# Kernel optimization log

Hardware: AMD Instinct MI355X
Metric: run time of the kernel (lower is better)

The kernel has to match this reference:

```python
import jax, jax.numpy as jnp
import numpy as np

N, C, WP, H, W = 2, 64, 64, 240, 320
NB, K = 6, 3  # num_bases, input_ks
EPS = 1e-5


def _conv(x, w, pad):
    return jax.lax.conv_general_dilated(
        x, w, (1, 1), [(pad, pad), (pad, pad)],
        dimension_numbers=('NCHW', 'OIHW', 'NCHW'))


def _bn(x, g, b, m, v):
    # eval-mode BatchNorm2d with running stats
    inv = g * jax.lax.rsqrt(v + EPS)
    return x * inv[None, :, None, None] + (b - m * inv)[None, :, None, None]


def _forward(feat, weight, w1, b1, w2, b2, coef, coef_bias,
             br_gamma, br_beta, br_mean, br_var,
             w3, bn3_gamma, bn3_beta, bn3_mean, bn3_var):
    n, c, h, w = feat.shape
    # conv_bases: Basic2d (3x3 conv + bias + relu) then 1x1 conv -> K*K*NB channels
    cat = jnp.concatenate([feat, weight], axis=1)
    t = jax.nn.relu(_conv(cat, w1, 1) + b1[None, :, None, None])
    bases = _conv(t, w2, 0) + b2[None, :, None, None]          # [N, NB*K*K, H, W]
    bases = bases.reshape(n, NB, K * K, h, w)                   # [N, NB, L, H, W]
    # F.unfold: im2col patches, channel-major (C outer, kh*kw inner) like torch
    patches = jax.lax.conv_general_dilated_patches(
        feat, (K, K), (1, 1), [(1, 1), (1, 1)],
        dimension_numbers=('NCHW', 'OIHW', 'NCHW'))             # [N, C*K*K, H, W]
    patches = patches.reshape(n, c, K * K, h, w)                # [N, C, L, H, W]
    # dynamic per-pixel basis combination
    bases_out = jnp.einsum('bmlhw,bclhw->bcmhw', bases, patches)
    bases_out = bases_out.reshape(n, c * NB, h, w)              # [N, C*NB, H, W]
    # 1x1 conv with coef + bias
    out = _conv(bases_out, coef, 0) + coef_bias[None, :, None, None]
    # br: BN + ReLU
    out = jax.nn.relu(_bn(out, br_gamma, br_beta, br_mean, br_var))
    # conv3: Basic2d with BN (3x3 conv no bias + BN + ReLU)
    out = _conv(out, w3, 1)
    out = jax.nn.relu(_bn(out, bn3_gamma, bn3_beta, bn3_mean, bn3_var))
    return out


def setup_inputs() -> dict:
    key = jax.random.key(0)
    ks = jax.random.split(key, 8)
    f = lambda i, s, sc: jax.random.normal(ks[i], s, dtype=jnp.float32) * sc
    return {
        'feat': f(0, (N, C, H, W), 1.0),
        'weight': f(1, (N, WP, H, W), 1.0),
        'w1': f(2, (C, C + WP, 3, 3), 0.05),
        'b1': jnp.zeros((C,), jnp.float32),
        'w2': f(3, (K * K * NB, C, 1, 1), 0.05),
        'b2': jnp.zeros((K * K * NB,), jnp.float32),
        'coef': f(4, (C, C * NB, 1, 1), 0.05),
        'coef_bias': jnp.zeros((C,), jnp.float32),
        'br_gamma': jnp.ones((C,), jnp.float32),
        'br_beta': jnp.zeros((C,), jnp.float32),
        'br_mean': jnp.zeros((C,), jnp.float32),
        'br_var': jnp.ones((C,), jnp.float32),
        'w3': f(5, (C, C, 3, 3), 0.05),
        'bn3_gamma': jnp.ones((C,), jnp.float32),
        'bn3_beta': jnp.zeros((C,), jnp.float32),
        'bn3_mean': jnp.zeros((C,), jnp.float32),
        'bn3_var': jnp.ones((C,), jnp.float32),
    }


def reference(feat, weight, w1, b1, w2, b2, coef, coef_bias,
              br_gamma, br_beta, br_mean, br_var,
              w3, bn3_gamma, bn3_beta, bn3_mean, bn3_var):
    return _forward(feat, weight, w1, b1, w2, b2, coef, coef_bias,
                    br_gamma, br_beta, br_mean, br_var,
                    w3, bn3_gamma, bn3_beta, bn3_mean, bn3_var)
```

## Files before the change

### kernel.cpp

```cpp
#include <hip/hip_runtime.h>
#include <math.h>

#define HH 240
#define WW 320
#define HWSZ (240*320)
#define NN 2

#define OFF_BW1   0
#define OFF_BW3   147456
#define OFF_W2A   221184
#define OFF_COEFA 229376
#define OFF_BN    278528
#define OFF_FHF   279552
#define OFF_FHW   19940352

typedef __attribute__((ext_vector_type(8))) _Float16 half8v;
typedef __attribute__((ext_vector_type(4))) _Float16 half4v;
typedef __attribute__((ext_vector_type(2))) _Float16 half2v;
typedef __attribute__((ext_vector_type(4))) float f32x4;

__device__ __forceinline__ half8v h8zero() {
    half8v z;
    #pragma unroll
    for (int j = 0; j < 8; ++j) z[j] = (_Float16)0.f;
    return z;
}

__device__ void do_prep(int id, const float* __restrict__ w1, const float* __restrict__ w3,
                        const float* __restrict__ w2, const float* __restrict__ coef,
                        const float* __restrict__ coef_bias,
                        const float* __restrict__ brg, const float* __restrict__ brb,
                        const float* __restrict__ brm, const float* __restrict__ brv,
                        const float* __restrict__ g3, const float* __restrict__ b3,
                        const float* __restrict__ m3, const float* __restrict__ v3,
                        float* __restrict__ ws) {
    _Float16* hw = (_Float16*)ws;

    if (id < 9216) {
        int l = id & 63; int f = id >> 6;
        int m = f & 3;   int g = f >> 2;
        int t = g % 9, cc = g / 9;
        _Float16* dst = hw + OFF_BW1/2 + (size_t)(g*4 + m)*512 + l*8;
        #pragma unroll
        for (int j = 0; j < 8; ++j) {
            int ci = cc*32 + (l>>4)*8 + j;
            int co = m*16 + (l&15);
            dst[j] = (_Float16)w1[(co*128 + ci)*9 + t];
        }
        return;
    }
    id -= 9216;
    if (id < 4608) {
        int l = id & 63; int f = id >> 6;
        int m = f & 3;   int g = f >> 2;
        int t = g % 9, cc = g / 9;
        _Float16* dst = hw + OFF_BW3/2 + (size_t)(g*4 + m)*512 + l*8;
        #pragma unroll
        for (int j = 0; j < 8; ++j) {
            int ci = cc*32 + (l>>4)*8 + j;
            int co = m*16 + (l&15);
            dst[j] = (_Float16)w3[(co*64 + ci)*9 + t];
        }
        return;
    }
    id -= 4608;
    if (id < 512) {
        int l = id & 63; int f = id >> 6;
        int mf = f & 3, kc = f >> 2;
        int row = mf*16 + (l & 15);
        _Float16* dst = hw + OFF_W2A/2 + (size_t)((kc*4 + mf)*64 + l)*8;
        #pragma unroll
        for (int j = 0; j < 8; ++j) {
            int k = kc*32 + (l>>4)*8 + j;
            dst[j] = (row < 54) ? (_Float16)w2[row*64 + k] : (_Float16)0.f;
        }
        return;
    }
    id -= 512;
    if (id < 3072) {
        int l = id & 63; int f = id >> 6;
        int ocf = f & 3; int g2 = f >> 2;
        int ch = g2 % 3, cg = g2 / 3;
        int oc = ocf*16 + (l & 15);
        _Float16* dst = hw + OFF_COEFA/2 + (size_t)((g2*4 + ocf)*64 + l)*8;
        #pragma unroll
        for (int j = 0; j < 8; ++j) {
            int k32 = (l>>4)*8 + j;
            int m = ch*2 + (k32 >> 4);
            int c = cg*16 + (k32 & 15);
            dst[j] = (_Float16)coef[oc*384 + c*6 + m];
        }
        return;
    }
    id -= 3072;
    if (id < 64) {
        float s = brg[id] * rsqrtf(brv[id] + 1e-5f);
        ws[OFF_BN/4 + id]      = s;
        ws[OFF_BN/4 + 64 + id] = coef_bias[id]*s + brb[id] - brm[id]*s;
        return;
    }
    id -= 64;
    if (id < 64) {
        float s = g3[id] * rsqrtf(v3[id] + 1e-5f);
        ws[OFF_BN/4 + 128 + id] = s;
        ws[OFF_BN/4 + 192 + id] = b3[id] - m3[id]*s;
    }
}

__global__ void nhwc_k(const float* __restrict__ feat, const float* __restrict__ wgt,
                       _Float16* __restrict__ fhf, _Float16* __restrict__ fhw,
                       const float* __restrict__ w1, const float* __restrict__ w3,
                       const float* __restrict__ w2, const float* __restrict__ coef,
                       const float* __restrict__ coef_bias,
                       const float* __restrict__ brg, const float* __restrict__ brb,
                       const float* __restrict__ brm, const float* __restrict__ brv,
                       const float* __restrict__ g3, const float* __restrict__ b3,
                       const float* __restrict__ m3, const float* __restrict__ v3,
                       float* __restrict__ ws) {
    __shared__ float L[64][65];
    const int tid = threadIdx.x;

    const int bid = blockIdx.y * 5 + blockIdx.x;
    if (blockIdx.z == 0 && bid < 69)
        do_prep(bid*256 + tid, w1, w3, w2, coef, coef_bias,
                brg, brb, brm, brv, g3, b3, m3, v3, ws);

    const int xb = blockIdx.x * 64, y = blockIdx.y;
    const int n = blockIdx.z >> 1, w = blockIdx.z & 1;
    const float* src = (w ? wgt : feat) + (size_t)n*64*HWSZ + y*WW + xb;
    _Float16* dst = (w ? fhw : fhf) + ((size_t)n*HWSZ + y*WW + xb) * 64;
    const int lx = tid & 63, c4 = tid >> 6;
    #pragma unroll
    for (int k = 0; k < 16; ++k) {
        int c = c4*16 + k;
        L[c][lx] = src[(size_t)c*HWSZ + lx];
    }
    __syncthreads();
    const int x = tid >> 3, c0 = (tid & 7) * 8;
    #pragma unroll
    for (int h = 0; h < 2; ++h) {
        int xx = x + h*32;
        half8v v;
        #pragma unroll
        for (int j = 0; j < 8; ++j) v[j] = (_Float16)L[c0 + j][xx];
        *(half8v*)&dst[xx*64 + c0] = v;
    }
}

template<int CHUNKS, bool HAS_SCALE>
__launch_bounds__(256, 1)
__global__ void convmfma_k(const _Float16* __restrict__ in0, const _Float16* __restrict__ in1,
                           const _Float16* __restrict__ wfr,
                           const float* __restrict__ epiA, const float* __restrict__ epiB,
                           float* __restrict__ outF, _Float16* __restrict__ outH) {
    __shared__ alignas(16) _Float16 TILE[2][180*40];
    const int tid = threadIdx.x;
    const int lane = tid & 63, wv = tid >> 6;
    const int l15 = lane & 15, l4 = lane >> 4;
    const int x0 = blockIdx.x * 16, y0 = blockIdx.y * 8;
    const int nb = blockIdx.z;
    const int NT = CHUNKS * 9;

    f32x4 acc[8];
    #pragma unroll
    for (int nf = 0; nf < 8; ++nf)
        acc[nf] = (f32x4){0.f, 0.f, 0.f, 0.f};

    half8v sv[3];
    auto issue = [&](int cc) {
        const _Float16* tens = (cc < 2) ? in0 : in1;
        const int choff = (cc & 1) * 32;
        const _Float16* base = tens + (size_t)nb * HWSZ * 64;
        #pragma unroll
        for (int it = 0; it < 3; ++it) {
            int task = tid + it*256;
            sv[it] = h8zero();
            if (it < 2 || task < 720) {
                int pos = task >> 2, hh = task & 3;
                int py = pos / 18, px = pos - py*18;
                int gy = y0 - 1 + py, gx = x0 - 1 + px;
                bool ok = (gy >= 0) & (gy < HH) & (gx >= 0) & (gx < WW);
                if (ok) sv[it] = *(const half8v*)&base[((size_t)(gy*WW + gx))*64 + choff + hh*8];
            }
        }
    };
    auto commit = [&](int buf) {
        #pragma unroll
        for (int it = 0; it < 3; ++it) {
            int task = tid + it*256;
            if (it < 2 || task < 720) {
                int pos = task >> 2, hh = task & 3;
                *(half8v*)&TILE[buf][pos*40 + hh*8] = sv[it];
            }
        }
    };

    half8v Wf[2];
    auto loadW = [&](int g, int b) {
        Wf[b] = *(const half8v*)(wfr + (size_t)(g*4 + wv)*512 + lane*8);
    };

    issue(0);
    commit(0);
    loadW(0, 0);
    __syncthreads();

    #pragma unroll
    for (int cc = 0; cc < CHUNKS; ++cc) {
        if (cc + 1 < CHUNKS) issue(cc + 1);
        const _Float16* Tc = &TILE[cc & 1][0];
        #pragma unroll
        for (int t = 0; t < 9; ++t) {
            const int g = cc*9 + t;
            const int b = g & 1;
            if (g + 1 < NT) loadW(g + 1, b ^ 1);
            const int ky = t / 3, kx = t - ky*3;
            #pragma unroll
            for (int nf = 0; nf < 8; ++nf) {
                int pos = (nf + ky)*18 + l15 + kx;
                half8v Ph = *(const half8v*)&Tc[pos*40 + l4*8];
                acc[nf] = __builtin_amdgcn_mfma_f32_16x16x32_f16(Wf[b], Ph, acc[nf], 0, 0, 0);
            }
        }
        if (cc + 1 < CHUNKS) {
            commit((cc + 1) & 1);
            __syncthreads();
        }
    }

    if (HAS_SCALE) {
        #pragma unroll
        for (int i = 0; i < 4; ++i) {
            int co = wv*16 + l4*4 + i;
            float sc = epiA[co], ofs = epiB[co];
            float* op = outF + (size_t)(nb*64 + co) * HWSZ;
            #pragma unroll
            for (int nf = 0; nf < 8; ++nf) {
                int y = y0 + nf, x = x0 + l15;
                op[y*WW + x] = fmaxf(acc[nf][i]*sc + ofs, 0.f);
            }
        }
    } else {
        #pragma unroll
        for (int nf = 0; nf < 8; ++nf) {
            int y = y0 + nf, x = x0 + l15;
            _Float16* op = outH + ((size_t)nb*HWSZ + y*WW + x) * 64;
            half4v hv;
            #pragma unroll
            for (int i = 0; i < 4; ++i) {
                float v = acc[nf][i] + epiA[wv*16 + l4*4 + i];
                hv[i] = (_Float16)fmaxf(v, 0.f);
            }
            *(half4v*)&op[wv*16 + l4*4] = hv;
        }
    }
}

__launch_bounds__(256, 1)
__global__ void fuse2_k(const _Float16* __restrict__ fhf, const _Float16* __restrict__ tH,
                        const _Float16* __restrict__ w2a,
                        const float* __restrict__ b2,
                        const _Float16* __restrict__ coefa,
                        const float* __restrict__ bn,
                        _Float16* __restrict__ uH) {
    __shared__ alignas(16) _Float16 BSH[128*72];
    __shared__ alignas(16) _Float16 PT[180*24];
    const int tid = threadIdx.x;
    const int lane = tid & 63, wv = tid >> 6;
    const int l15 = lane & 15, l4 = lane >> 4;
    const int x0 = blockIdx.x*16, y0 = blockIdx.y*8;
    const int nb = blockIdx.z;

    int s_pos[2], s_gy[2], s_gx[2], s_oct[2];
    bool s_ok[2], s_act[2];
    #pragma unroll
    for (int it = 0; it < 2; ++it) {
        int task = tid + it*256;
        s_act[it] = (task < 360);
        int pos = task >> 1, oct = task & 1;
        int py = pos / 18, pxx = pos - py*18;
        int gy = y0 - 1 + py, gx = x0 - 1 + pxx;
        s_pos[it] = pos; s_oct[it] = oct;
        s_gy[it] = gy; s_gx[it] = gx;
        s_ok[it] = (gy >= 0) & (gy < HH) & (gx >= 0) & (gx < WW) & s_act[it];
    }
    const _Float16* fbase = fhf + (size_t)nb * HWSZ * 64;

    half8v sv0 = h8zero(), sv1 = h8zero();
    if (s_ok[0]) sv0 = *(const half8v*)&fbase[((size_t)(s_gy[0]*WW + s_gx[0]))*64 + s_oct[0]*8];
    if (s_ok[1]) sv1 = *(const half8v*)&fbase[((size_t)(s_gy[1]*WW + s_gx[1]))*64 + s_oct[1]*8];

    half8v w2f[2][4];
    #pragma unroll
    for (int kc = 0; kc < 2; ++kc)
        #pragma unroll
        for (int mf = 0; mf < 4; ++mf)
            w2f[kc][mf] = *(const half8v*)(w2a + (size_t)((kc*4 + mf)*64 + lane)*8);

    f32x4 b2v[4];
    #pragma unroll
    for (int mf = 0; mf < 4; ++mf)
        #pragma unroll
        for (int i = 0; i < 4; ++i) {
            int row = mf*16 + l4*4 + i;
            b2v[mf][i] = (row < 54) ? b2[row] : 0.f;
        }

    #pragma unroll
    for (int nf = 0; nf < 2; ++nf) {
        int r = wv*2 + nf;
        int y = y0 + r, x = x0 + l15;
        const _Float16* tp = tH + ((size_t)nb*HWSZ + y*WW + x) * 64;
        half8v tf0 = *(const half8v*)&tp[l4*8];
        half8v tf1 = *(const half8v*)&tp[32 + l4*8];
        int px = r*16 + l15;
        #pragma unroll
        for (int mf = 0; mf < 4; ++mf) {
            f32x4 ab = (f32x4){0.f, 0.f, 0.f, 0.f};
            ab = __builtin_amdgcn_mfma_f32_16x16x32_f16(w2f[0][mf], tf0, ab, 0, 0, 0);
            ab = __builtin_amdgcn_mfma_f32_16x16x32_f16(w2f[1][mf], tf1, ab, 0, 0, 0);
            if (mf < 3 || l4 < 2) {
                #pragma unroll
                for (int i = 0; i < 4; ++i) {
                    int jb = mf*16 + l4*4 + i;
                    int m = jb / 9;
                    int tap = jb - m*9;
                    BSH[px*72 + tap*8 + (m & 1)*4 + (m >> 1)] = (_Float16)(ab[i] + b2v[mf][i]);
                }
            }
        }
    }

    const int m0 = l4 >> 1;
    const int c08 = (l4 & 1) * 8;
    #pragma unroll
    for (int it = 0; it < 2; ++it) {
        if (s_act[it])
            *(half8v*)&PT[s_pos[it]*24 + s_oct[it]*8] = (it ? sv1 : sv0);
    }
    __syncthreads();

    f32x4 acc[4][2];
    #pragma unroll
    for (int m = 0; m < 4; ++m)
        #pragma unroll
        for (int nf = 0; nf < 2; ++nf)
            acc[m][nf] = (f32x4){0.f, 0.f, 0.f, 0.f};

    #pragma unroll 1
    for (int cg = 0; cg < 4; ++cg) {
        half8v nv0 = h8zero(), nv1 = h8zero();
        if (cg < 3) {
            int chb = (cg + 1)*16;
            if (s_ok[0]) nv0 = *(const half8v*)&fbase[((size_t)(s_gy[0]*WW + s_gx[0]))*64 + chb + s_oct[0]*8];
            if (s_ok[1]) nv1 = *(const half8v*)&fbase[((size_t)(s_gy[1]*WW + s_gx[1]))*64 + chb + s_oct[1]*8];
        }

        #pragma unroll
        for (int nf = 0; nf < 2; ++nf) {
            int r = wv*2 + nf;
            int px = r*16 + l15;
            half2v s2[3][4];
            #pragma unroll
            for (int ch = 0; ch < 3; ++ch)
                #pragma unroll
                for (int q = 0; q < 4; ++q)
                    s2[ch][q] = (half2v){(_Float16)0.f, (_Float16)0.f};

            #pragma unroll
            for (int tap = 0; tap < 9; ++tap) {
                int ky = tap / 3, kx = tap - ky*3;
                int pos = (r + ky)*18 + l15 + kx;
                half8v pt = *(const half8v*)&PT[pos*24 + c08];
                half4v bv = *(const half4v*)&BSH[px*72 + tap*8 + m0*4];
                half2v b0 = (half2v){bv[0], bv[0]};
                half2v b1 = (half2v){bv[1], bv[1]};
                half2v bx = (half2v){bv[2], bv[2]};
                #pragma unroll
                for (int q = 0; q < 4; ++q) {
                    half2v pq = (half2v){pt[2*q], pt[2*q + 1]};
                    s2[0][q] = pq * b0 + s2[0][q];
                    s2[1][q] = pq * b1 + s2[1][q];
                    s2[2][q] = pq * bx + s2[2][q];
                }
            }
            half8v B0, B1, B2;
            #pragma unroll
            for (int q = 0; q < 4; ++q) {
                B0[2*q] = s2[0][q][0]; B0[2*q+1] = s2[0][q][1];
                B1[2*q] = s2[1][q][0]; B1[2*q+1] = s2[1][q][1];
                B2[2*q] = s2[2][q][0]; B2[2*q+1] = s2[2][q][1];
            }
            #pragma unroll
            for (int hf = 0; hf < 2; ++hf) {
                half8v CAh[3][2];
                #pragma unroll
                for (int ch = 0; ch < 3; ++ch)
                    #pragma unroll
                    for (int o = 0; o < 2; ++o)
                        CAh[ch][o] = *(const half8v*)(coefa +
                            (size_t)(((cg*3 + ch)*4 + hf*2 + o)*64 + lane)*8);
                #pragma unroll
                for (int o = 0; o < 2; ++o) {
                    int oc = hf*2 + o;
                    acc[oc][nf] = __builtin_amdgcn_mfma_f32_16x16x32_f16(CAh[0][o], B0, acc[oc][nf], 0, 0, 0);
                    acc[oc][nf] = __builtin_amdgcn_mfma_f32_16x16x32_f16(CAh[1][o], B1, acc[oc][nf], 0, 0, 0);
                    acc[oc][nf] = __builtin_amdgcn_mfma_f32_16x16x32_f16(CAh[2][o], B2, acc[oc][nf], 0, 0, 0);
                }
            }
        }

        if (cg < 3) {
            __syncthreads();
            #pragma unroll
            for (int it = 0; it < 2; ++it) {
                if (s_act[it])
                    *(half8v*)&PT[s_pos[it]*24 + s_oct[it]*8] = (it ? nv1 : nv0);
            }
            __syncthreads();
        }
    }

    #pragma unroll
    for (int nf = 0; nf < 2; ++nf) {
        int y = y0 + wv*2 + nf, x = x0 + l15;
        _Float16* up = uH + ((size_t)nb*HWSZ + y*WW + x) * 64;
        #pragma unroll
        for (int ocf = 0; ocf < 4; ++ocf) {
            half4v hv;
            #pragma unroll
            for (int i = 0; i < 4; ++i) {
                int co = ocf*16 + l4*4 + i;
                hv[i] = (_Float16)fmaxf(acc[ocf][nf][i]*bn[co] + bn[64 + co], 0.f);
            }
            *(half4v*)&up[ocf*16 + l4*4] = hv;
        }
    }
}

extern "C" void kernel_launch(void* const* d_in, const int* in_sizes, int n_in,
                              void* d_out, int out_size, void* d_ws, size_t ws_size,
                              hipStream_t stream) {
    const float* feat      = (const float*)d_in[0];
    const float* wgt       = (const float*)d_in[1];
    const float* w1        = (const float*)d_in[2];
    const float* b1        = (const float*)d_in[3];
    const float* w2        = (const float*)d_in[4];
    const float* b2        = (const float*)d_in[5];
    const float* coef      = (const float*)d_in[6];
    const float* coef_bias = (const float*)d_in[7];
    const float* brg       = (const float*)d_in[8];
    const float* brb       = (const float*)d_in[9];
    const float* brm       = (const float*)d_in[10];
    const float* brv       = (const float*)d_in[11];
    const float* w3        = (const float*)d_in[12];
    const float* g3        = (const float*)d_in[13];
    const float* b3        = (const float*)d_in[14];
    const float* m3        = (const float*)d_in[15];
    const float* v3        = (const float*)d_in[16];

    float* out = (float*)d_out;
    _Float16* tH = (_Float16*)d_out;
    float* ws  = (float*)d_ws;
    _Float16* hw = (_Float16*)ws;
    _Float16* FHf = hw + OFF_FHF/2;
    _Float16* FHw = hw + OFF_FHW/2;

    nhwc_k<<<dim3(5, 240, 4), 256, 0, stream>>>(feat, wgt, FHf, FHw,
        w1, w3, w2, coef, coef_bias, brg, brb, brm, brv, g3, b3, m3, v3, ws);

    dim3 grid(WW/16, HH/8, NN);

    convmfma_k<4, false><<<grid, 256, 0, stream>>>(
        FHf, FHw, hw + OFF_BW1/2, b1, b1, nullptr, tH);

    fuse2_k<<<grid, 256, 0, stream>>>(FHf, tH,
        hw + OFF_W2A/2, b2, hw + OFF_COEFA/2, ws + OFF_BN/4, FHw);

    convmfma_k<2, true><<<grid, 256, 0, stream>>>(
        FHw, FHw, hw + OFF_BW3/2,
        ws + OFF_BN/4 + 128, ws + OFF_BN/4 + 192, out, nullptr);
}
```

Before: 104.5 us.

## Fuse first 3x3 conv with bases/dynamic-combine stage into one kernel

Adds a kernel that computes the first 3x3 conv (ReLU) tile-wise into shared memory and immediately feeds it into the 1x1 bases conv, per-pixel basis combination and coef 1x1 conv with BN+ReLU. This removes the intermediate t tensor round-trip through global memory and one kernel launch. It writes the result to a new workspace region and only runs when the workspace is large enough, otherwise falling back to the old three-kernel path. Shared memory is reused across phases, which adds extra barriers and higher register pressure.

Result: faster. 100.0 us, median of 2 (-4.3%).

```diff
diff --git a/kernel.cpp b/kernel.cpp
--- a/kernel.cpp
+++ b/kernel.cpp
@@ -13,6 +13,8 @@
 #define OFF_BN    278528
 #define OFF_FHF   279552
 #define OFF_FHW   19940352
+#define OFF_U     39601152
+#define WS_FUSED  (OFF_U + 19660800)
 
 typedef __attribute__((ext_vector_type(8))) _Float16 half8v;
 typedef __attribute__((ext_vector_type(4))) _Float16 half4v;
@@ -144,6 +146,271 @@
         #pragma unroll
         for (int j = 0; j < 8; ++j) v[j] = (_Float16)L[c0 + j][xx];
         *(half8v*)&dst[xx*64 + c0] = v;
+    }
+}
+
+__launch_bounds__(256, 1)
+__global__ void c1f2_k(const _Float16* __restrict__ fhf, const _Float16* __restrict__ fhw,
+                       const _Float16* __restrict__ wfr, const float* __restrict__ b1,
+                       const _Float16* __restrict__ w2a, const float* __restrict__ b2,
+                       const _Float16* __restrict__ coefa, const float* __restrict__ bn,
+                       _Float16* __restrict__ uH) {
+    __shared__ alignas(16) char SMEM[35840];
+    _Float16* TILEa = (_Float16*)SMEM;
+    _Float16* tL    = (_Float16*)SMEM;
+    _Float16* PT    = (_Float16*)SMEM;
+    _Float16* BSH   = (_Float16*)(SMEM + 17408);
+
+    const int tid = threadIdx.x;
+    const int lane = tid & 63, wv = tid >> 6;
+    const int l15 = lane & 15, l4 = lane >> 4;
+    const int x0 = blockIdx.x * 16, y0 = blockIdx.y * 8;
+    const int nb = blockIdx.z;
+
+    f32x4 cacc[8];
+    #pragma unroll
+    for (int nf = 0; nf < 8; ++nf)
+        cacc[nf] = (f32x4){0.f, 0.f, 0.f, 0.f};
+
+    half8v sv[3];
+    auto issue = [&](int cc) {
+        const _Float16* tens = (cc < 2) ? fhf : fhw;
+        const int choff = (cc & 1) * 32;
+        const _Float16* base = tens + (size_t)nb * HWSZ * 64;
+        #pragma unroll
+        for (int it = 0; it < 3; ++it) {
+            int task = tid + it*256;
+            sv[it] = h8zero();
+            if (it < 2 || task < 720) {
+                int pos = task >> 2, hh = task & 3;
+                int py = pos / 18, px = pos - py*18;
+                int gy = y0 - 1 + py, gx = x0 - 1 + px;
+                bool ok = (gy >= 0) & (gy < HH) & (gx >= 0) & (gx < WW);
+                if (ok) sv[it] = *(const half8v*)&base[((size_t)(gy*WW + gx))*64 + choff + hh*8];
+            }
+        }
+    };
+    auto commit = [&](int buf) {
+        #pragma unroll
+        for (int it = 0; it < 3; ++it) {
+            int task = tid + it*256;
+            if (it < 2 || task < 720) {
+                int pos = task >> 2, hh = task & 3;
+                *(half8v*)&TILEa[buf*7200 + pos*40 + hh*8] = sv[it];
+            }
+        }
+    };
+
+    half8v Wf[2];
+    auto loadW = [&](int g, int b) {
+        Wf[b] = *(const half8v*)(wfr + (size_t)(g*4 + wv)*512 + lane*8);
+    };
+
+    issue(0);
+    commit(0);
+    loadW(0, 0);
+    __syncthreads();
+
+    #pragma unroll
+    for (int cc = 0; cc < 4; ++cc) {
+        if (cc + 1 < 4) issue(cc + 1);
+        const _Float16* Tc = &TILEa[(cc & 1)*7200];
+        #pragma unroll
+        for (int t = 0; t < 9; ++t) {
+            const int g = cc*9 + t;
+            const int b = g & 1;
+            if (g + 1 < 36) loadW(g + 1, b ^ 1);
+            const int ky = t / 3, kx = t - ky*3;
+            #pragma unroll
+            for (int nf = 0; nf < 8; ++nf) {
+                int pos = (nf + ky)*18 + l15 + kx;
+                half8v Ph = *(const half8v*)&Tc[pos*40 + l4*8];
+                cacc[nf] = __builtin_amdgcn_mfma_f32_16x16x32_f16(Wf[b], Ph, cacc[nf], 0, 0, 0);
+            }
+        }
+        if (cc + 1 < 4) {
+            commit((cc + 1) & 1);
+            __syncthreads();
+        }
+    }
+
+    __syncthreads();
+    float bch[4];
+    #pragma unroll
+    for (int i = 0; i < 4; ++i) bch[i] = b1[wv*16 + l4*4 + i];
+    #pragma unroll
+    for (int nf = 0; nf < 8; ++nf) {
+        half4v hv;
+        #pragma unroll
+        for (int i = 0; i < 4; ++i)
+            hv[i] = (_Float16)fmaxf(cacc[nf][i] + bch[i], 0.f);
+        *(half4v*)&tL[(nf*16 + l15)*68 + wv*16 + l4*4] = hv;
+    }
+    __syncthreads();
+
+    half8v w2f[2][4];
+    #pragma unroll
+    for (int kc = 0; kc < 2; ++kc)
+        #pragma unroll
+        for (int mf = 0; mf < 4; ++mf)
+            w2f[kc][mf] = *(const half8v*)(w2a + (size_t)((kc*4 + mf)*64 + lane)*8);
+
+    f32x4 b2v[4];
+    #pragma unroll
+    for (int mf = 0; mf < 4; ++mf)
+        #pragma unroll
+        for (int i = 0; i < 4; ++i) {
+            int row = mf*16 + l4*4 + i;
+            b2v[mf][i] = (row < 54) ? b2[row] : 0.f;
+        }
+
+    int s_pos[2], s_gy[2], s_gx[2], s_oct[2];
+    bool s_ok[2], s_act[2];
+    #pragma unroll
+    for (int it = 0; it < 2; ++it) {
+        int task = tid + it*256;
+        s_act[it] = (task < 360);
+        int pos = task >> 1, oct = task & 1;
+        int py = pos / 18, pxx = pos - py*18;
+        int gy = y0 - 1 + py, gx = x0 - 1 + pxx;
+        s_pos[it] = pos; s_oct[it] = oct;
+        s_gy[it] = gy; s_gx[it] = gx;
+        s_ok[it] = (gy >= 0) & (gy < HH) & (gx >= 0) & (gx < WW) & s_act[it];
+    }
+    const _Float16* fbase = fhf + (size_t)nb * HWSZ * 64;
+    half8v sv0 = h8zero(), sv1 = h8zero();
+    if (s_ok[0]) sv0 = *(const half8v*)&fbase[((size_t)(s_gy[0]*WW + s_gx[0]))*64 + s_oct[0]*8];
+    if (s_ok[1]) sv1 = *(const half8v*)&fbase[((size_t)(s_gy[1]*WW + s_gx[1]))*64 + s_oct[1]*8];
+
+    #pragma unroll
+    for (int nf = 0; nf < 2; ++nf) {
+        int r = wv*2 + nf;
+        int px = r*16 + l15;
+        half8v tf0 = *(const half8v*)&tL[px*68 + l4*8];
+        half8v tf1 = *(const half8v*)&tL[px*68 + 32 + l4*8];
+        #pragma unroll
+        for (int mf = 0; mf < 4; ++mf) {
+            f32x4 ab = (f32x4){0.f, 0.f, 0.f, 0.f};
+            ab = __builtin_amdgcn_mfma_f32_16x16x32_f16(w2f[0][mf], tf0, ab, 0, 0, 0);
+            ab = __builtin_amdgcn_mfma_f32_16x16x32_f16(w2f[1][mf], tf1, ab, 0, 0, 0);
+            if (mf < 3 || l4 < 2) {
+                #pragma unroll
+                for (int i = 0; i < 4; ++i) {
+                    int jb = mf*16 + l4*4 + i;
+                    int m = jb / 9;
+                    int tap = jb - m*9;
+                    BSH[px*72 + tap*8 + (m & 1)*4 + (m >> 1)] = (_Float16)(ab[i] + b2v[mf][i]);
+                }
+            }
+        }
+    }
+
+    __syncthreads();
+
+    const int m0 = l4 >> 1;
+    const int c08 = (l4 & 1) * 8;
+    #pragma unroll
+    for (int it = 0; it < 2; ++it) {
+        if (s_act[it])
+            *(half8v*)&PT[s_pos[it]*24 + s_oct[it]*8] = (it ? sv1 : sv0);
+    }
+    __syncthreads();
+
+    f32x4 acc[4][2];
+    #pragma unroll
+    for (int m = 0; m < 4; ++m)
+        #pragma unroll
+        for (int nf = 0; nf < 2; ++nf)
+            acc[m][nf] = (f32x4){0.f, 0.f, 0.f, 0.f};
+
+    #pragma unroll 1
+    for (int cg = 0; cg < 4; ++cg) {
+        half8v nv0 = h8zero(), nv1 = h8zero();
+        if (cg < 3) {
+            int chb = (cg + 1)*16;
+            if (s_ok[0]) nv0 = *(const half8v*)&fbase[((size_t)(s_gy[0]*WW + s_gx[0]))*64 + chb + s_oct[0]*8];
+            if (s_ok[1]) nv1 = *(const half8v*)&fbase[((size_t)(s_gy[1]*WW + s_gx[1]))*64 + chb + s_oct[1]*8];
+        }
+
+        #pragma unroll
+        for (int nf = 0; nf < 2; ++nf) {
+            int r = wv*2 + nf;
+            int px = r*16 + l15;
+            half2v s2[3][4];
+            #pragma unroll
+            for (int ch = 0; ch < 3; ++ch)
+                #pragma unroll
+                for (int q = 0; q < 4; ++q)
+                    s2[ch][q] = (half2v){(_Float16)0.f, (_Float16)0.f};
+
+            #pragma unroll
+            for (int tap = 0; tap < 9; ++tap) {
+                int ky = tap / 3, kx = tap - ky*3;
+                int pos = (r + ky)*18 + l15 + kx;
+                half8v pt = *(const half8v*)&PT[pos*24 + c08];
+                half4v bv = *(const half4v*)&BSH[px*72 + tap*8 + m0*4];
+                half2v b0 = (half2v){bv[0], bv[0]};
+                half2v b1h = (half2v){bv[1], bv[1]};
+                half2v bx = (half2v){bv[2], bv[2]};
+                #pragma unroll
+                for (int q = 0; q < 4; ++q) {
+                    half2v pq = (half2v){pt[2*q], pt[2*q + 1]};
+                    s2[0][q] = pq * b0 + s2[0][q];
+                    s2[1][q] = pq * b1h + s2[1][q];
+                    s2[2][q] = pq * bx + s2[2][q];
+                }
+            }
+            half8v B0, B1, B2;
+            #pragma unroll
+            for (int q = 0; q < 4; ++q) {
+                B0[2*q] = s2[0][q][0]; B0[2*q+1] = s2[0][q][1];
+                B1[2*q] = s2[1][q][0]; B1[2*q+1] = s2[1][q][1];
+                B2[2*q] = s2[2][q][0]; B2[2*q+1] = s2[2][q][1];
+            }
+            #pragma unroll
+            for (int hf = 0; hf < 2; ++hf) {
+                half8v CAh[3][2];
+                #pragma unroll
+                for (int ch = 0; ch < 3; ++ch)
+                    #pragma unroll
+                    for (int o = 0; o < 2; ++o)
+                        CAh[ch][o] = *(const half8v*)(coefa +
+                            (size_t)(((cg*3 + ch)*4 + hf*2 + o)*64 + lane)*8);
+                #pragma unroll
+                for (int o = 0; o < 2; ++o) {
+                    int oc = hf*2 + o;
+                    acc[oc][nf] = __builtin_amdgcn_mfma_f32_16x16x32_f16(CAh[0][o], B0, acc[oc][nf], 0, 0, 0);
+                    acc[oc][nf] = __builtin_amdgcn_mfma_f32_16x16x32_f16(CAh[1][o], B1, acc[oc][nf], 0, 0, 0);
+                    acc[oc][nf] = __builtin_amdgcn_mfma_f32_16x16x32_f16(CAh[2][o], B2, acc[oc][nf], 0, 0, 0);
+                }
+            }
+        }
+
+        if (cg < 3) {
+            __syncthreads();
+            #pragma unroll
+            for (int it = 0; it < 2; ++it) {
+                if (s_act[it])
+                    *(half8v*)&PT[s_pos[it]*24 + s_oct[it]*8] = (it ? nv1 : nv0);
+            }
+            __syncthreads();
+        }
+    }
+
+    #pragma unroll
+    for (int nf = 0; nf < 2; ++nf) {
+        int y = y0 + wv*2 + nf, x = x0 + l15;
+        _Float16* up = uH + ((size_t)nb*HWSZ + y*WW + x) * 64;
+        #pragma unroll
+        for (int ocf = 0; ocf < 4; ++ocf) {
+            half4v hv;
+            #pragma unroll
+            for (int i = 0; i < 4; ++i) {
+                int co = ocf*16 + l4*4 + i;
+                hv[i] = (_Float16)fmaxf(acc[ocf][nf][i]*bn[co] + bn[64 + co], 0.f);
+            }
+            *(half4v*)&up[ocf*16 + l4*4] = hv;
+        }
     }
 }
 
@@ -471,13 +738,20 @@
 
     dim3 grid(WW/16, HH/8, NN);
 
-    convmfma_k<4, false><<<grid, 256, 0, stream>>>(
-        FHf, FHw, hw + OFF_BW1/2, b1, b1, nullptr, tH);
-
-    fuse2_k<<<grid, 256, 0, stream>>>(FHf, tH,
-        hw + OFF_W2A/2, b2, hw + OFF_COEFA/2, ws + OFF_BN/4, FHw);
-
-    convmfma_k<2, true><<<grid, 256, 0, stream>>>(
-        FHw, FHw, hw + OFF_BW3/2,
-        ws + OFF_BN/4 + 128, ws + OFF_BN/4 + 192, out, nullptr);
+    if (ws_size >= (size_t)WS_FUSED) {
+        _Float16* U = hw + OFF_U/2;
+        c1f2_k<<<grid, 256, 0, stream>>>(FHf, FHw, hw + OFF_BW1/2, b1,
+            hw + OFF_W2A/2, b2, hw + OFF_COEFA/2, ws + OFF_BN/4, U);
+        convmfma_k<2, true><<<grid, 256, 0, stream>>>(
+            U, U, hw + OFF_BW3/2,
+            ws + OFF_BN/4 + 128, ws + OFF_BN/4 + 192, out, nullptr);
+    } else {
+        convmfma_k<4, false><<<grid, 256, 0, stream>>>(
+            FHf, FHw, hw + OFF_BW1/2, b1, b1, nullptr, tH);
+        fuse2_k<<<grid, 256, 0, stream>>>(FHf, tH,
+            hw + OFF_W2A/2, b2, hw + OFF_COEFA/2, ws + OFF_BN/4, FHw);
+        convmfma_k<2, true><<<grid, 256, 0, stream>>>(
+            FHw, FHw, hw + OFF_BW3/2,
+            ws + OFF_BN/4 + 128, ws + OFF_BN/4 + 192, out, nullptr);
+    }
 }
```
